# Optimization experiments

Measured on AMD Instinct MI355X. Metric: run time of the kernel, lower is better.

Reference implementation:

```python
import jax, jax.numpy as jnp
import numpy as np

N_NODES = 50000
N_EDGES = 800000
F_IN = 128
LN_EPS = 1e-5


def _linear_params(key, fan_in, fan_out):
    kw, kb = jax.random.split(key)
    w = jax.random.normal(kw, (fan_in, fan_out), dtype=jnp.float32) * 0.02
    b = jax.random.normal(kb, (fan_out,), dtype=jnp.float32) * 0.02
    return w, b


def setup_inputs() -> dict:
    key = jax.random.key(0)
    ks = jax.random.split(key, 16)
    x = jax.random.normal(ks[0], (N_NODES, F_IN), dtype=jnp.float32)
    edge_index = jax.random.randint(ks[1], (2, N_EDGES), 0, N_NODES, dtype=jnp.int32)
    w1a, b1a = _linear_params(ks[2], F_IN, 256)
    w1b, b1b = _linear_params(ks[3], 256, 256)
    w2a, b2a = _linear_params(ks[4], 256, 512)
    w2b, b2b = _linear_params(ks[5], 512, 512)
    w3a, b3a = _linear_params(ks[6], 512, 1024)
    w3b, b3b = _linear_params(ks[7], 1024, 1024)
    rp1_w, rp1_b = _linear_params(ks[8], F_IN, 256)
    rp2_w, rp2_b = _linear_params(ks[9], 256, 512)
    rp3_w, rp3_b = _linear_params(ks[10], 512, 1024)
    ln1_g = jnp.ones((256,), jnp.float32); ln1_b = jnp.zeros((256,), jnp.float32)
    ln2_g = jnp.ones((512,), jnp.float32); ln2_b = jnp.zeros((512,), jnp.float32)
    ln3_g = jnp.ones((1024,), jnp.float32); ln3_b = jnp.zeros((1024,), jnp.float32)
    return dict(x=x, edge_index=edge_index,
                w1a=w1a, b1a=b1a, w1b=w1b, b1b=b1b,
                w2a=w2a, b2a=b2a, w2b=w2b, b2b=b2b,
                w3a=w3a, b3a=b3a, w3b=w3b, b3b=b3b,
                rp1_w=rp1_w, rp1_b=rp1_b, rp2_w=rp2_w, rp2_b=rp2_b,
                rp3_w=rp3_w, rp3_b=rp3_b,
                ln1_g=ln1_g, ln1_b=ln1_b, ln2_g=ln2_g, ln2_b=ln2_b,
                ln3_g=ln3_g, ln3_b=ln3_b)


def _layer_norm(h, g, b):
    mu = jnp.mean(h, axis=-1, keepdims=True)
    var = jnp.mean(jnp.square(h - mu), axis=-1, keepdims=True)
    return (h - mu) * jax.lax.rsqrt(var + LN_EPS) * g + b


def _gin_conv(h, src, dst, wa, ba, wb, bb):
    # GINConv with eps=0: mlp(x_i + sum_{j->i} x_j), scatter-add at targets
    agg = jax.ops.segment_sum(h[src], dst, num_segments=N_NODES)
    z = h + agg
    z = jax.nn.relu(z @ wa + ba)
    z = jax.nn.relu(z @ wb + bb)
    return z


def _forward(x, edge_index,
             w1a, b1a, w1b, b1b, w2a, b2a, w2b, b2b, w3a, b3a, w3b, b3b,
             rp1_w, rp1_b, rp2_w, rp2_b, rp3_w, rp3_b,
             ln1_g, ln1_b, ln2_g, ln2_b, ln3_g, ln3_b):
    src, dst = edge_index[0], edge_index[1]
    # block 1
    res = x @ rp1_w + rp1_b
    h = _gin_conv(x, src, dst, w1a, b1a, w1b, b1b)
    h = jax.nn.relu(h + res)          # dropout = identity in eval
    h = _layer_norm(h, ln1_g, ln1_b)
    # block 2
    res = h @ rp2_w + rp2_b
    h2 = _gin_conv(h, src, dst, w2a, b2a, w2b, b2b)
    h = jax.nn.relu(h2 + res)
    h = _layer_norm(h, ln2_g, ln2_b)
    # block 3
    res = h @ rp3_w + rp3_b
    h3 = _gin_conv(h, src, dst, w3a, b3a, w3b, b3b)
    h = jax.nn.relu(h3 + res)
    h = _layer_norm(h, ln3_g, ln3_b)
    return h


def reference(x, edge_index,
              w1a, b1a, w1b, b1b, w2a, b2a, w2b, b2b, w3a, b3a, w3b, b3b,
              rp1_w, rp1_b, rp2_w, rp2_b, rp3_w, rp3_b,
              ln1_g, ln1_b, ln2_g, ln2_b, ln3_g, ln3_b):
    return _forward(x, edge_index,
                    w1a, b1a, w1b, b1b, w2a, b2a, w2b, b2b, w3a, b3a, w3b, b3b,
                    rp1_w, rp1_b, rp2_w, rp2_b, rp3_w, rp3_b,
                    ln1_g, ln1_b, ln2_g, ln2_b, ln3_g, ln3_b)
```

## Files before the change

kernel.cpp:

```cpp
#include <hip/hip_runtime.h>
#include <stdint.h>

#define NN 50000
#define NE 800000
#define M_PAD 50048

typedef __attribute__((ext_vector_type(8))) short short8;
typedef __attribute__((ext_vector_type(4))) float f32x4;

static __device__ __forceinline__ float bf2f(unsigned short v) {
    union { unsigned u; float f; } c; c.u = ((unsigned)v) << 16; return c.f;
}
static __device__ __forceinline__ unsigned short f2bf(float f) {
    union { float f; unsigned u; } c; c.f = f;
    unsigned u = c.u;
    u += 0x7fffu + ((u >> 16) & 1u);
    return (unsigned short)(u >> 16);
}

__global__ void f32_to_bf16_k(const float* __restrict__ in, unsigned short* __restrict__ out, long n4) {
    long i = (long)blockIdx.x * 256 + threadIdx.x;
    if (i >= n4) return;
    float4 v = ((const float4*)in)[i];
    ushort4 o; o.x = f2bf(v.x); o.y = f2bf(v.y); o.z = f2bf(v.z); o.w = f2bf(v.w);
    ((ushort4*)out)[i] = o;
}
__global__ void wt_k(const float* __restrict__ w, unsigned short* __restrict__ wt, int K, int N) {
    int i = blockIdx.x * 256 + threadIdx.x;
    if (i >= K * N) return;
    int k = i % K, n = i / K;
    wt[i] = f2bf(w[(long)k * N + n]);
}

__global__ void zero_k(int* __restrict__ p, int n) {
    int i = blockIdx.x * 256 + threadIdx.x;
    if (i < n) p[i] = 0;
}
__global__ void hist_k(const int* __restrict__ ei, int* __restrict__ deg) {
    int e = blockIdx.x * 256 + threadIdx.x;
    if (e >= NE) return;
    atomicAdd(&deg[ei[NE + e]], 1);
}
__global__ __launch_bounds__(1024)
void scan_k(const int* __restrict__ deg, int* __restrict__ row_ptr, int* __restrict__ cursor) {
    constexpr int T = 1024, C = (NN + T - 1) / T;
    const int tid = threadIdx.x;
    const int base = tid * C;
    int s = 0;
#pragma unroll 4
    for (int i = 0; i < C; ++i) {
        int idx = base + i;
        if (idx < NN) s += deg[idx];
    }
    __shared__ int sm[T];
    sm[tid] = s;
    __syncthreads();
    for (int off = 1; off < T; off <<= 1) {
        int v = (tid >= off) ? sm[tid - off] : 0;
        __syncthreads();
        sm[tid] += v;
        __syncthreads();
    }
    int run = (tid == 0) ? 0 : sm[tid - 1];
#pragma unroll 4
    for (int i = 0; i < C; ++i) {
        int idx = base + i;
        if (idx < NN) {
            row_ptr[idx] = run;
            cursor[idx] = run;
            run += deg[idx];
        }
    }
}
__global__ void build_col_k(const int* __restrict__ ei, int* __restrict__ cursor, int* __restrict__ col) {
    int e = blockIdx.x * 256 + threadIdx.x;
    if (e >= NE) return;
    int d = ei[NE + e];
    int p = atomicAdd(&cursor[d], 1);
    col[p] = ei[e];
}

template <int V> struct VecT;
template <> struct VecT<2> { using T = unsigned int; };
template <> struct VecT<4> { using T = uint2; };
template <> struct VecT<8> { using T = uint4; };

template <int D>
__global__ __launch_bounds__(256)
void agg_gather_k(const unsigned short* __restrict__ h,
                  const int* __restrict__ row_ptr, const int* __restrict__ deg,
                  const int* __restrict__ col, unsigned short* __restrict__ z) {
    constexpr int V = D / 64;
    using VT = typename VecT<V>::T;
    union U { VT v; unsigned short s[V]; };
    const int node = blockIdx.x * 4 + (threadIdx.x >> 6);
    if (node >= NN) return;
    const int lane = threadIdx.x & 63;
    const size_t fb = (size_t)lane * V;

    float acc[V];
    {
        U b; b.v = *(const VT*)(h + (size_t)node * D + fb);
#pragma unroll
        for (int i = 0; i < V; ++i) acc[i] = bf2f(b.s[i]);
    }
    const int s = row_ptr[node];
    const int e = s + deg[node];
    int t = s;
    for (; t + 2 <= e; t += 2) {
        int s0 = col[t], s1 = col[t + 1];
        U a0, a1;
        a0.v = *(const VT*)(h + (size_t)s0 * D + fb);
        a1.v = *(const VT*)(h + (size_t)s1 * D + fb);
#pragma unroll
        for (int i = 0; i < V; ++i) acc[i] += bf2f(a0.s[i]);
#pragma unroll
        for (int i = 0; i < V; ++i) acc[i] += bf2f(a1.s[i]);
    }
    if (t < e) {
        U a; a.v = *(const VT*)(h + (size_t)col[t] * D + fb);
#pragma unroll
        for (int i = 0; i < V; ++i) acc[i] += bf2f(a.s[i]);
    }
    U o;
#pragma unroll
    for (int i = 0; i < V; ++i) o.s[i] = f2bf(acc[i]);
    *(VT*)(z + (size_t)node * D + fb) = o.v;
}

static __device__ __forceinline__ void stage_tile128x64(
    const unsigned short* __restrict__ src, size_t rstride,
    unsigned short* lds, int wid, int lane) {
#pragma unroll
    for (int r = 0; r < 4; ++r) {
        const int rows8 = wid * 32 + r * 8;
        const int row = rows8 + (lane >> 3);
        const int kblk = (lane & 7) ^ (row & 7);
        __builtin_amdgcn_global_load_lds(
            (const __attribute__((address_space(1))) void*)(src + (size_t)row * rstride + (size_t)kblk * 8),
            (__attribute__((address_space(3))) void*)(lds + rows8 * 64),
            16, 0, 0);
    }
}

#define GEMM_IDS(NT)                                                      \
    const int tid = threadIdx.x;                                          \
    const int lane = tid & 63;                                            \
    const int wid = tid >> 6;                                             \
    const int wm = wid & 1, wn = wid >> 1;                                \
    const int l15 = lane & 15, quad = lane >> 4;                          \
    int m0, n0;                                                           \
    {                                                                     \
        const int nwg = (int)(gridDim.x * gridDim.y);                     \
        const int orig = (int)(blockIdx.y * gridDim.x + blockIdx.x);      \
        const int q = nwg >> 3, r = nwg & 7;                              \
        const int xcd = orig & 7, idx = orig >> 3;                        \
        const int logical =                                               \
            (xcd < r ? xcd * (q + 1) : r * (q + 1) + (xcd - r) * q) + idx;\
        m0 = (logical / (NT)) * 128;                                      \
        n0 = (logical % (NT)) * 128;                                      \
    }

#define GEMM_KSTEP(AP, BP, KS)                                                        \
    for (int k0 = 0; k0 < (KS); k0 += 64) {                                           \
        stage_tile128x64((AP) + (size_t)m0 * (KS) + k0, (KS), lA, wid, lane);         \
        stage_tile128x64((BP) + (size_t)n0 * (KS) + k0, (KS), lB, wid, lane);         \
        __syncthreads();                                                              \
        _Pragma("unroll")                                                             \
        for (int kk = 0; kk < 2; ++kk) {                                              \
            short8 aF[4], bF[4];                                                      \
            _Pragma("unroll")                                                         \
            for (int i = 0; i < 4; ++i) {                                             \
                int ml = wm * 64 + i * 16 + l15;                                      \
                int kb = kk * 4 + quad;                                               \
                aF[i] = *(const short8*)&lA[(ml * 8 + (kb ^ (ml & 7))) * 8];          \
                int nl = wn * 64 + i * 16 + l15;                                      \
                bF[i] = *(const short8*)&lB[(nl * 8 + (kb ^ (nl & 7))) * 8];          \
            }                                                                         \
            _Pragma("unroll")                                                         \
            for (int i = 0; i < 4; ++i)                                               \
                _Pragma("unroll")                                                     \
                for (int j = 0; j < 4; ++j)                                           \
                    acc[i][j] = __builtin_amdgcn_mfma_f32_16x16x32_bf16(              \
                        aF[i], bF[j], acc[i][j], 0, 0, 0);                            \
        }                                                                             \
        __syncthreads();                                                              \
    }

template <int K, int N>
__global__ __launch_bounds__(256, 2)
void gemm_relu_k(const unsigned short* __restrict__ A, const unsigned short* __restrict__ Bt,
                 const float* __restrict__ bias, unsigned short* __restrict__ outH, int M) {
    __shared__ unsigned short lA[128 * 64];
    __shared__ unsigned short lB[128 * 64];
    GEMM_IDS(N / 128)
    f32x4 acc[4][4];
#pragma unroll
    for (int i = 0; i < 4; ++i)
#pragma unroll
        for (int j = 0; j < 4; ++j) acc[i][j] = (f32x4){0.f, 0.f, 0.f, 0.f};

    GEMM_KSTEP(A, Bt, K)

#pragma unroll
    for (int i = 0; i < 4; ++i) {
#pragma unroll
        for (int j = 0; j < 4; ++j) {
            int col = n0 + wn * 64 + j * 16 + l15;
            float bv = bias[col];
#pragma unroll
            for (int r = 0; r < 4; ++r) {
                int row = m0 + wm * 64 + i * 16 + quad * 4 + r;
                if (row < M)
                    outH[(size_t)row * N + col] = f2bf(fmaxf(acc[i][j][r] + bv, 0.f));
            }
        }
    }
}

template <int K1, int K2, int N>
__global__ __launch_bounds__(256, 2)
void gemm_fused_k(const unsigned short* __restrict__ A1, const unsigned short* __restrict__ B1t,
                  const float* __restrict__ b1,
                  const unsigned short* __restrict__ A2, const unsigned short* __restrict__ B2t,
                  const float* __restrict__ b2,
                  float* __restrict__ outF, int M) {
    __shared__ unsigned short lA[128 * 64];
    __shared__ unsigned short lB[128 * 64];
    GEMM_IDS(N / 128)
    f32x4 acc[4][4];
#pragma unroll
    for (int i = 0; i < 4; ++i)
#pragma unroll
        for (int j = 0; j < 4; ++j) acc[i][j] = (f32x4){0.f, 0.f, 0.f, 0.f};

    GEMM_KSTEP(A1, B1t, K1)

#pragma unroll
    for (int j = 0; j < 4; ++j) {
        float bv = b1[n0 + wn * 64 + j * 16 + l15];
#pragma unroll
        for (int i = 0; i < 4; ++i)
#pragma unroll
            for (int r = 0; r < 4; ++r)
                acc[i][j][r] = fmaxf(acc[i][j][r] + bv, 0.f);
    }

    GEMM_KSTEP(A2, B2t, K2)

#pragma unroll
    for (int i = 0; i < 4; ++i) {
#pragma unroll
        for (int j = 0; j < 4; ++j) {
            int col = n0 + wn * 64 + j * 16 + l15;
            float bv = b2[col];
#pragma unroll
            for (int r = 0; r < 4; ++r) {
                int row = m0 + wm * 64 + i * 16 + quad * 4 + r;
                if (row < M)
                    outF[(size_t)row * N + col] = fmaxf(acc[i][j][r] + bv, 0.f);
            }
        }
    }
}

template <int D, bool BF16OUT>
__global__ __launch_bounds__(256)
void ln_k(const float* __restrict__ t, const float* __restrict__ g, const float* __restrict__ b,
          unsigned short* __restrict__ outH, float* __restrict__ outF) {
    constexpr int VPT = D / 256;
    const int row = blockIdx.x;
    const int tid = threadIdx.x;
    const float* tp = t + (size_t)row * D;
    float vals[VPT];
    float s = 0.f, ss = 0.f;
#pragma unroll
    for (int i = 0; i < VPT; ++i) {
        float v = tp[i * 256 + tid];
        vals[i] = v; s += v; ss += v * v;
    }
#pragma unroll
    for (int off = 32; off; off >>= 1) { s += __shfl_down(s, off); ss += __shfl_down(ss, off); }
    __shared__ float ps[4], pss[4];
    int lane = tid & 63, wv = tid >> 6;
    if (lane == 0) { ps[wv] = s; pss[wv] = ss; }
    __syncthreads();
    float st = ps[0] + ps[1] + ps[2] + ps[3];
    float sst = pss[0] + pss[1] + pss[2] + pss[3];
    float mean = st / D;
    float var = sst / D - mean * mean;
    float inv = rsqrtf(var + 1e-5f);
#pragma unroll
    for (int i = 0; i < VPT; ++i) {
        int c = i * 256 + tid;
        float o = (vals[i] - mean) * inv * g[c] + b[c];
        if (BF16OUT) outH[(size_t)row * D + c] = f2bf(o);
        else outF[(size_t)row * D + c] = o;
    }
}

static inline int cdiv(long a, long b) { return (int)((a + b - 1) / b); }

extern "C" void kernel_launch(void* const* d_in, const int* in_sizes, int n_in,
                              void* d_out, int out_size, void* d_ws, size_t ws_size,
                              hipStream_t stream) {
    const float* x   = (const float*)d_in[0];
    const int*   ei  = (const int*)  d_in[1];
    const float* w1a = (const float*)d_in[2],  *b1a = (const float*)d_in[3];
    const float* w1b = (const float*)d_in[4],  *b1b = (const float*)d_in[5];
    const float* w2a = (const float*)d_in[6],  *b2a = (const float*)d_in[7];
    const float* w2b = (const float*)d_in[8],  *b2b = (const float*)d_in[9];
    const float* w3a = (const float*)d_in[10], *b3a = (const float*)d_in[11];
    const float* w3b = (const float*)d_in[12], *b3b = (const float*)d_in[13];
    const float* rp1 = (const float*)d_in[14], *rp1b = (const float*)d_in[15];
    const float* rp2 = (const float*)d_in[16], *rp2b = (const float*)d_in[17];
    const float* rp3 = (const float*)d_in[18], *rp3b = (const float*)d_in[19];
    const float* g1 = (const float*)d_in[20], *be1 = (const float*)d_in[21];
    const float* g2 = (const float*)d_in[22], *be2 = (const float*)d_in[23];
    const float* g3 = (const float*)d_in[24], *be3 = (const float*)d_in[25];

    char* ws = (char*)d_ws;
    size_t off = 0;
    auto alloc = [&](size_t n) { char* p = ws + off; off += (n + 255) & ~(size_t)255; return p; };
    unsigned short* w1aT = (unsigned short*)alloc((size_t)128 * 256 * 2);
    unsigned short* w1bT = (unsigned short*)alloc((size_t)256 * 256 * 2);
    unsigned short* w2aT = (unsigned short*)alloc((size_t)256 * 512 * 2);
    unsigned short* w2bT = (unsigned short*)alloc((size_t)512 * 512 * 2);
    unsigned short* w3aT = (unsigned short*)alloc((size_t)512 * 1024 * 2);
    unsigned short* w3bT = (unsigned short*)alloc((size_t)1024 * 1024 * 2);
    unsigned short* rp1T = (unsigned short*)alloc((size_t)128 * 256 * 2);
    unsigned short* rp2T = (unsigned short*)alloc((size_t)256 * 512 * 2);
    unsigned short* rp3T = (unsigned short*)alloc((size_t)512 * 1024 * 2);
    unsigned short* hA  = (unsigned short*)alloc((size_t)M_PAD * 512 * 2);
    unsigned short* hB  = (unsigned short*)alloc((size_t)M_PAD * 512 * 2);
    unsigned short* zin = (unsigned short*)alloc((size_t)M_PAD * 512 * 2);
    unsigned short* z1  = (unsigned short*)alloc((size_t)M_PAD * 1024 * 2);
    float* resb = (float*)alloc((size_t)M_PAD * 1024 * 4);
    int* deg     = (int*)alloc((size_t)NN * 4);
    int* row_ptr = (int*)alloc((size_t)NN * 4);
    int* cursor  = (int*)alloc((size_t)NN * 4);
    int* colv    = (int*)alloc((size_t)NE * 4);
    (void)ws_size; (void)in_sizes; (void)n_in; (void)out_size;

    zero_k<<<cdiv(NN, 256), 256, 0, stream>>>(deg, NN);
    hist_k<<<cdiv(NE, 256), 256, 0, stream>>>(ei, deg);
    scan_k<<<1, 1024, 0, stream>>>(deg, row_ptr, cursor);
    build_col_k<<<cdiv(NE, 256), 256, 0, stream>>>(ei, cursor, colv);

    wt_k<<<cdiv(128 * 256, 256), 256, 0, stream>>>(w1a, w1aT, 128, 256);
    wt_k<<<cdiv(256 * 256, 256), 256, 0, stream>>>(w1b, w1bT, 256, 256);
    wt_k<<<cdiv(256 * 512, 256), 256, 0, stream>>>(w2a, w2aT, 256, 512);
    wt_k<<<cdiv(512 * 512, 256), 256, 0, stream>>>(w2b, w2bT, 512, 512);
    wt_k<<<cdiv(512 * 1024, 256), 256, 0, stream>>>(w3a, w3aT, 512, 1024);
    wt_k<<<cdiv(1024 * 1024, 256), 256, 0, stream>>>(w3b, w3bT, 1024, 1024);
    wt_k<<<cdiv(128 * 256, 256), 256, 0, stream>>>(rp1, rp1T, 128, 256);
    wt_k<<<cdiv(256 * 512, 256), 256, 0, stream>>>(rp2, rp2T, 256, 512);
    wt_k<<<cdiv(512 * 1024, 256), 256, 0, stream>>>(rp3, rp3T, 512, 1024);

    f32_to_bf16_k<<<cdiv((long)NN * 128 / 4, 256), 256, 0, stream>>>(x, hA, (long)NN * 128 / 4);

    agg_gather_k<128><<<cdiv(NN, 4), 256, 0, stream>>>(hA, row_ptr, deg, colv, zin);
    gemm_relu_k<128, 256><<<dim3(2, 391), 256, 0, stream>>>(zin, w1aT, b1a, z1, NN);
    gemm_fused_k<256, 128, 256><<<dim3(2, 391), 256, 0, stream>>>(z1, w1bT, b1b, hA, rp1T, rp1b, resb, NN);
    ln_k<256, true><<<NN, 256, 0, stream>>>(resb, g1, be1, hB, nullptr);

    agg_gather_k<256><<<cdiv(NN, 4), 256, 0, stream>>>(hB, row_ptr, deg, colv, zin);
    gemm_relu_k<256, 512><<<dim3(4, 391), 256, 0, stream>>>(zin, w2aT, b2a, z1, NN);
    gemm_fused_k<512, 256, 512><<<dim3(4, 391), 256, 0, stream>>>(z1, w2bT, b2b, hB, rp2T, rp2b, resb, NN);
    ln_k<512, true><<<NN, 256, 0, stream>>>(resb, g2, be2, hA, nullptr);

    agg_gather_k<512><<<cdiv(NN, 4), 256, 0, stream>>>(hA, row_ptr, deg, colv, zin);
    gemm_relu_k<512, 1024><<<dim3(8, 391), 256, 0, stream>>>(zin, w3aT, b3a, z1, NN);
    gemm_fused_k<1024, 512, 1024><<<dim3(8, 391), 256, 0, stream>>>(z1, w3bT, b3b, hA, rp3T, rp3b, resb, NN);
    ln_k<1024, false><<<NN, 256, 0, stream>>>(resb, g3, be3, nullptr, (float*)d_out);
}
```

Measured before the change: 1.257 ms.

## Double-buffer GEMM LDS tiles and store bf16 pre-LayerNorm activations

Replaces the single-buffered k-loop with a two-stage LDS ping-pong so the next 128x64 tiles load while MFMAs run on the current ones, with one barrier per step. The fused GEMM also gains a bf16 output mode that blocks 1 and 2 use for the residual sum, so LayerNorm reads half the bytes. Double-buffering doubles LDS use to 64KB per block, which may limit occupancy. The bf16 intermediate adds rounding before normalisation.

After: 1.417 ms. +12.8%, slower.

```diff
diff --git a/kernel.cpp b/kernel.cpp
--- a/kernel.cpp
+++ b/kernel.cpp
@@ -161,38 +161,50 @@
         n0 = (logical % (NT)) * 128;                                      \
     }
 
-#define GEMM_KSTEP(AP, BP, KS)                                                        \
-    for (int k0 = 0; k0 < (KS); k0 += 64) {                                           \
-        stage_tile128x64((AP) + (size_t)m0 * (KS) + k0, (KS), lA, wid, lane);         \
-        stage_tile128x64((BP) + (size_t)n0 * (KS) + k0, (KS), lB, wid, lane);         \
-        __syncthreads();                                                              \
-        _Pragma("unroll")                                                             \
-        for (int kk = 0; kk < 2; ++kk) {                                              \
-            short8 aF[4], bF[4];                                                      \
-            _Pragma("unroll")                                                         \
-            for (int i = 0; i < 4; ++i) {                                             \
-                int ml = wm * 64 + i * 16 + l15;                                      \
-                int kb = kk * 4 + quad;                                               \
-                aF[i] = *(const short8*)&lA[(ml * 8 + (kb ^ (ml & 7))) * 8];          \
-                int nl = wn * 64 + i * 16 + l15;                                      \
-                bF[i] = *(const short8*)&lB[(nl * 8 + (kb ^ (nl & 7))) * 8];          \
+#define GEMM_PIPE(AP, BP, KS)                                                         \
+    {                                                                                 \
+        stage_tile128x64((AP) + (size_t)m0 * (KS), (KS), &lA[0][0], wid, lane);       \
+        stage_tile128x64((BP) + (size_t)n0 * (KS), (KS), &lB[0][0], wid, lane);       \
+        asm volatile("s_waitcnt vmcnt(0)" ::: "memory");                              \
+        __builtin_amdgcn_s_barrier();                                                 \
+        const int NT_ = (KS) / 64;                                                    \
+        for (int t = 0; t < NT_; ++t) {                                               \
+            const int cb = t & 1;                                                     \
+            if (t + 1 < NT_) {                                                        \
+                stage_tile128x64((AP) + (size_t)m0 * (KS) + (size_t)(t + 1) * 64,     \
+                                 (KS), &lA[cb ^ 1][0], wid, lane);                    \
+                stage_tile128x64((BP) + (size_t)n0 * (KS) + (size_t)(t + 1) * 64,     \
+                                 (KS), &lB[cb ^ 1][0], wid, lane);                    \
             }                                                                         \
             _Pragma("unroll")                                                         \
-            for (int i = 0; i < 4; ++i)                                               \
+            for (int kk = 0; kk < 2; ++kk) {                                          \
+                short8 aF[4], bF[4];                                                  \
                 _Pragma("unroll")                                                     \
-                for (int j = 0; j < 4; ++j)                                           \
-                    acc[i][j] = __builtin_amdgcn_mfma_f32_16x16x32_bf16(              \
-                        aF[i], bF[j], acc[i][j], 0, 0, 0);                            \
+                for (int i = 0; i < 4; ++i) {                                         \
+                    int ml = wm * 64 + i * 16 + l15;                                  \
+                    int kb = kk * 4 + quad;                                           \
+                    aF[i] = *(const short8*)&lA[cb][(ml * 8 + (kb ^ (ml & 7))) * 8];  \
+                    int nl = wn * 64 + i * 16 + l15;                                  \
+                    bF[i] = *(const short8*)&lB[cb][(nl * 8 + (kb ^ (nl & 7))) * 8];  \
+                }                                                                     \
+                _Pragma("unroll")                                                     \
+                for (int i = 0; i < 4; ++i)                                           \
+                    _Pragma("unroll")                                                 \
+                    for (int j = 0; j < 4; ++j)                                       \
+                        acc[i][j] = __builtin_amdgcn_mfma_f32_16x16x32_bf16(          \
+                            aF[i], bF[j], acc[i][j], 0, 0, 0);                        \
+            }                                                                         \
+            asm volatile("s_waitcnt vmcnt(0)" ::: "memory");                          \
+            __builtin_amdgcn_s_barrier();                                             \
         }                                                                             \
-        __syncthreads();                                                              \
     }
 
 template <int K, int N>
 __global__ __launch_bounds__(256, 2)
 void gemm_relu_k(const unsigned short* __restrict__ A, const unsigned short* __restrict__ Bt,
                  const float* __restrict__ bias, unsigned short* __restrict__ outH, int M) {
-    __shared__ unsigned short lA[128 * 64];
-    __shared__ unsigned short lB[128 * 64];
+    __shared__ unsigned short lA[2][128 * 64];
+    __shared__ unsigned short lB[2][128 * 64];
     GEMM_IDS(N / 128)
     f32x4 acc[4][4];
 #pragma unroll
@@ -200,7 +212,7 @@
 #pragma unroll
         for (int j = 0; j < 4; ++j) acc[i][j] = (f32x4){0.f, 0.f, 0.f, 0.f};
 
-    GEMM_KSTEP(A, Bt, K)
+    GEMM_PIPE(A, Bt, K)
 
 #pragma unroll
     for (int i = 0; i < 4; ++i) {
@@ -218,15 +230,15 @@
     }
 }
 
-template <int K1, int K2, int N>
+template <int K1, int K2, int N, bool OUTBF16>
 __global__ __launch_bounds__(256, 2)
 void gemm_fused_k(const unsigned short* __restrict__ A1, const unsigned short* __restrict__ B1t,
                   const float* __restrict__ b1,
                   const unsigned short* __restrict__ A2, const unsigned short* __restrict__ B2t,
                   const float* __restrict__ b2,
-                  float* __restrict__ outF, int M) {
-    __shared__ unsigned short lA[128 * 64];
-    __shared__ unsigned short lB[128 * 64];
+                  unsigned short* __restrict__ outH, float* __restrict__ outF, int M) {
+    __shared__ unsigned short lA[2][128 * 64];
+    __shared__ unsigned short lB[2][128 * 64];
     GEMM_IDS(N / 128)
     f32x4 acc[4][4];
 #pragma unroll
@@ -234,19 +246,22 @@
 #pragma unroll
         for (int j = 0; j < 4; ++j) acc[i][j] = (f32x4){0.f, 0.f, 0.f, 0.f};
 
-    GEMM_KSTEP(A1, B1t, K1)
+    float bmid[4];
+#pragma unroll
+    for (int j = 0; j < 4; ++j) bmid[j] = b1[n0 + wn * 64 + j * 16 + l15];
+
+    GEMM_PIPE(A1, B1t, K1)
 
 #pragma unroll
     for (int j = 0; j < 4; ++j) {
-        float bv = b1[n0 + wn * 64 + j * 16 + l15];
 #pragma unroll
         for (int i = 0; i < 4; ++i)
 #pragma unroll
             for (int r = 0; r < 4; ++r)
-                acc[i][j][r] = fmaxf(acc[i][j][r] + bv, 0.f);
-    }
-
-    GEMM_KSTEP(A2, B2t, K2)
+                acc[i][j][r] = fmaxf(acc[i][j][r] + bmid[j], 0.f);
+    }
+
+    GEMM_PIPE(A2, B2t, K2)
 
 #pragma unroll
     for (int i = 0; i < 4; ++i) {
@@ -257,26 +272,30 @@
 #pragma unroll
             for (int r = 0; r < 4; ++r) {
                 int row = m0 + wm * 64 + i * 16 + quad * 4 + r;
-                if (row < M)
-                    outF[(size_t)row * N + col] = fmaxf(acc[i][j][r] + bv, 0.f);
+                if (row < M) {
+                    float v = fmaxf(acc[i][j][r] + bv, 0.f);
+                    if constexpr (OUTBF16) outH[(size_t)row * N + col] = f2bf(v);
+                    else                   outF[(size_t)row * N + col] = v;
+                }
             }
         }
     }
 }
 
-template <int D, bool BF16OUT>
+template <int D, bool INBF16, bool BF16OUT>
 __global__ __launch_bounds__(256)
-void ln_k(const float* __restrict__ t, const float* __restrict__ g, const float* __restrict__ b,
+void ln_k(const unsigned short* __restrict__ tH, const float* __restrict__ tF,
+          const float* __restrict__ g, const float* __restrict__ b,
           unsigned short* __restrict__ outH, float* __restrict__ outF) {
     constexpr int VPT = D / 256;
     const int row = blockIdx.x;
     const int tid = threadIdx.x;
-    const float* tp = t + (size_t)row * D;
     float vals[VPT];
     float s = 0.f, ss = 0.f;
 #pragma unroll
     for (int i = 0; i < VPT; ++i) {
-        float v = tp[i * 256 + tid];
+        int c = i * 256 + tid;
+        float v = INBF16 ? bf2f(tH[(size_t)row * D + c]) : tF[(size_t)row * D + c];
         vals[i] = v; s += v; ss += v * v;
     }
 #pragma unroll
@@ -361,16 +380,19 @@
 
     agg_gather_k<128><<<cdiv(NN, 4), 256, 0, stream>>>(hA, row_ptr, deg, colv, zin);
     gemm_relu_k<128, 256><<<dim3(2, 391), 256, 0, stream>>>(zin, w1aT, b1a, z1, NN);
-    gemm_fused_k<256, 128, 256><<<dim3(2, 391), 256, 0, stream>>>(z1, w1bT, b1b, hA, rp1T, rp1b, resb, NN);
-    ln_k<256, true><<<NN, 256, 0, stream>>>(resb, g1, be1, hB, nullptr);
+    gemm_fused_k<256, 128, 256, true><<<dim3(2, 391), 256, 0, stream>>>(
+        z1, w1bT, b1b, hA, rp1T, rp1b, zin, nullptr, NN);
+    ln_k<256, true, true><<<NN, 256, 0, stream>>>(zin, nullptr, g1, be1, hB, nullptr);
 
     agg_gather_k<256><<<cdiv(NN, 4), 256, 0, stream>>>(hB, row_ptr, deg, colv, zin);
     gemm_relu_k<256, 512><<<dim3(4, 391), 256, 0, stream>>>(zin, w2aT, b2a, z1, NN);
-    gemm_fused_k<512, 256, 512><<<dim3(4, 391), 256, 0, stream>>>(z1, w2bT, b2b, hB, rp2T, rp2b, resb, NN);
-    ln_k<512, true><<<NN, 256, 0, stream>>>(resb, g2, be2, hA, nullptr);
+    gemm_fused_k<512, 256, 512, true><<<dim3(4, 391), 256, 0, stream>>>(
+        z1, w2bT, b2b, hB, rp2T, rp2b, zin, nullptr, NN);
+    ln_k<512, true, true><<<NN, 256, 0, stream>>>(zin, nullptr, g2, be2, hA, nullptr);
 
     agg_gather_k<512><<<cdiv(NN, 4), 256, 0, stream>>>(hA, row_ptr, deg, colv, zin);
     gemm_relu_k<512, 1024><<<dim3(8, 391), 256, 0, stream>>>(zin, w3aT, b3a, z1, NN);
-    gemm_fused_k<1024, 512, 1024><<<dim3(8, 391), 256, 0, stream>>>(z1, w3bT, b3b, hA, rp3T, rp3b, resb, NN);
-    ln_k<1024, false><<<NN, 256, 0, stream>>>(resb, g3, be3, nullptr, (float*)d_out);
-}
+    gemm_fused_k<1024, 512, 1024, false><<<dim3(8, 391), 256, 0, stream>>>(
+        z1, w3bT, b3b, hA, rp3T, rp3b, nullptr, resb, NN);
+    ln_k<1024, false, false><<<NN, 256, 0, stream>>>(nullptr, resb, g3, be3, nullptr, (float*)d_out);
+}
```

## Store pre-LN residual in bf16 for early blocks, vectorize LN and tiled weight transpose

Applied to the files above, without the earlier changes.

Blocks 1 and 2 now write the fused GEMM output as bf16 into a reused buffer instead of fp32, and layer norm reads bf16 input. This halves the intermediate traffic between GEMM and LN. LN loads and stores are vectorized per thread over contiguous columns. Weight transposes use a shared-memory 32x32 tile so both reads and writes are coalesced, and the mid bias is loaded before the first K loop. Rounding the pre-LN values to bf16 adds some precision loss.

Result: no change. 1.268 ms (+0.9%).

```diff
diff --git a/kernel.cpp b/kernel.cpp
--- a/kernel.cpp
+++ b/kernel.cpp
@@ -25,11 +25,18 @@
     ushort4 o; o.x = f2bf(v.x); o.y = f2bf(v.y); o.z = f2bf(v.z); o.w = f2bf(v.w);
     ((ushort4*)out)[i] = o;
 }
-__global__ void wt_k(const float* __restrict__ w, unsigned short* __restrict__ wt, int K, int N) {
-    int i = blockIdx.x * 256 + threadIdx.x;
-    if (i >= K * N) return;
-    int k = i % K, n = i / K;
-    wt[i] = f2bf(w[(long)k * N + n]);
+__global__ __launch_bounds__(256)
+void wt_k(const float* __restrict__ w, unsigned short* __restrict__ wt, int K, int N) {
+    __shared__ unsigned short t[32][33];
+    const int bk = blockIdx.y * 32, bn = blockIdx.x * 32;
+    const int tx = threadIdx.x & 31, ty = threadIdx.x >> 5;
+#pragma unroll
+    for (int r = 0; r < 32; r += 8)
+        t[ty + r][tx] = f2bf(w[(size_t)(bk + ty + r) * N + bn + tx]);
+    __syncthreads();
+#pragma unroll
+    for (int r = 0; r < 32; r += 8)
+        wt[(size_t)(bn + ty + r) * K + bk + tx] = t[tx][ty + r];
 }
 
 __global__ void zero_k(int* __restrict__ p, int n) {
@@ -218,13 +225,13 @@
     }
 }
 
-template <int K1, int K2, int N>
+template <int K1, int K2, int N, bool OUTBF16>
 __global__ __launch_bounds__(256, 2)
 void gemm_fused_k(const unsigned short* __restrict__ A1, const unsigned short* __restrict__ B1t,
                   const float* __restrict__ b1,
                   const unsigned short* __restrict__ A2, const unsigned short* __restrict__ B2t,
                   const float* __restrict__ b2,
-                  float* __restrict__ outF, int M) {
+                  unsigned short* __restrict__ outH, float* __restrict__ outF, int M) {
     __shared__ unsigned short lA[128 * 64];
     __shared__ unsigned short lB[128 * 64];
     GEMM_IDS(N / 128)
@@ -234,16 +241,19 @@
 #pragma unroll
         for (int j = 0; j < 4; ++j) acc[i][j] = (f32x4){0.f, 0.f, 0.f, 0.f};
 
+    float bmid[4];
+#pragma unroll
+    for (int j = 0; j < 4; ++j) bmid[j] = b1[n0 + wn * 64 + j * 16 + l15];
+
     GEMM_KSTEP(A1, B1t, K1)
 
 #pragma unroll
     for (int j = 0; j < 4; ++j) {
-        float bv = b1[n0 + wn * 64 + j * 16 + l15];
 #pragma unroll
         for (int i = 0; i < 4; ++i)
 #pragma unroll
             for (int r = 0; r < 4; ++r)
-                acc[i][j][r] = fmaxf(acc[i][j][r] + bv, 0.f);
+                acc[i][j][r] = fmaxf(acc[i][j][r] + bmid[j], 0.f);
     }
 
     GEMM_KSTEP(A2, B2t, K2)
@@ -257,28 +267,44 @@
 #pragma unroll
             for (int r = 0; r < 4; ++r) {
                 int row = m0 + wm * 64 + i * 16 + quad * 4 + r;
-                if (row < M)
-                    outF[(size_t)row * N + col] = fmaxf(acc[i][j][r] + bv, 0.f);
+                if (row < M) {
+                    float v = fmaxf(acc[i][j][r] + bv, 0.f);
+                    if constexpr (OUTBF16) outH[(size_t)row * N + col] = f2bf(v);
+                    else                   outF[(size_t)row * N + col] = v;
+                }
             }
         }
     }
 }
 
-template <int D, bool BF16OUT>
+template <int D, bool INBF16, bool BF16OUT>
 __global__ __launch_bounds__(256)
-void ln_k(const float* __restrict__ t, const float* __restrict__ g, const float* __restrict__ b,
+void ln_k(const unsigned short* __restrict__ tH, const float* __restrict__ tF,
+          const float* __restrict__ g, const float* __restrict__ b,
           unsigned short* __restrict__ outH, float* __restrict__ outF) {
     constexpr int VPT = D / 256;
     const int row = blockIdx.x;
     const int tid = threadIdx.x;
-    const float* tp = t + (size_t)row * D;
+    const int c0 = tid * VPT;
     float vals[VPT];
+    if constexpr (INBF16) {
+        const unsigned short* p = tH + (size_t)row * D + c0;
+        if constexpr (VPT == 1) { vals[0] = bf2f(p[0]); }
+        else if constexpr (VPT == 2) {
+            ushort2 u = *(const ushort2*)p; vals[0] = bf2f(u.x); vals[1] = bf2f(u.y);
+        } else {
+            ushort4 u = *(const ushort4*)p;
+            vals[0] = bf2f(u.x); vals[1] = bf2f(u.y); vals[2] = bf2f(u.z); vals[3] = bf2f(u.w);
+        }
+    } else {
+        const float* p = tF + (size_t)row * D + c0;
+        if constexpr (VPT == 1) { vals[0] = p[0]; }
+        else if constexpr (VPT == 2) { float2 u = *(const float2*)p; vals[0] = u.x; vals[1] = u.y; }
+        else { float4 u = *(const float4*)p; vals[0] = u.x; vals[1] = u.y; vals[2] = u.z; vals[3] = u.w; }
+    }
     float s = 0.f, ss = 0.f;
 #pragma unroll
-    for (int i = 0; i < VPT; ++i) {
-        float v = tp[i * 256 + tid];
-        vals[i] = v; s += v; ss += v * v;
-    }
+    for (int i = 0; i < VPT; ++i) { s += vals[i]; ss += vals[i] * vals[i]; }
 #pragma unroll
     for (int off = 32; off; off >>= 1) { s += __shfl_down(s, off); ss += __shfl_down(ss, off); }
     __shared__ float ps[4], pss[4];
@@ -290,12 +316,24 @@
     float mean = st / D;
     float var = sst / D - mean * mean;
     float inv = rsqrtf(var + 1e-5f);
-#pragma unroll
-    for (int i = 0; i < VPT; ++i) {
-        int c = i * 256 + tid;
-        float o = (vals[i] - mean) * inv * g[c] + b[c];
-        if (BF16OUT) outH[(size_t)row * D + c] = f2bf(o);
-        else outF[(size_t)row * D + c] = o;
+    float outv[VPT];
+#pragma unroll
+    for (int i = 0; i < VPT; ++i)
+        outv[i] = (vals[i] - mean) * inv * g[c0 + i] + b[c0 + i];
+    if constexpr (BF16OUT) {
+        unsigned short* p = outH + (size_t)row * D + c0;
+        if constexpr (VPT == 1) { p[0] = f2bf(outv[0]); }
+        else if constexpr (VPT == 2) {
+            ushort2 u; u.x = f2bf(outv[0]); u.y = f2bf(outv[1]); *(ushort2*)p = u;
+        } else {
+            ushort4 u; u.x = f2bf(outv[0]); u.y = f2bf(outv[1]); u.z = f2bf(outv[2]); u.w = f2bf(outv[3]);
+            *(ushort4*)p = u;
+        }
+    } else {
+        float* p = outF + (size_t)row * D + c0;
+        if constexpr (VPT == 1) { p[0] = outv[0]; }
+        else if constexpr (VPT == 2) { float2 u; u.x = outv[0]; u.y = outv[1]; *(float2*)p = u; }
+        else { float4 u; u.x = outv[0]; u.y = outv[1]; u.z = outv[2]; u.w = outv[3]; *(float4*)p = u; }
     }
 }
 
@@ -347,30 +385,33 @@
     scan_k<<<1, 1024, 0, stream>>>(deg, row_ptr, cursor);
     build_col_k<<<cdiv(NE, 256), 256, 0, stream>>>(ei, cursor, colv);
 
-    wt_k<<<cdiv(128 * 256, 256), 256, 0, stream>>>(w1a, w1aT, 128, 256);
-    wt_k<<<cdiv(256 * 256, 256), 256, 0, stream>>>(w1b, w1bT, 256, 256);
-    wt_k<<<cdiv(256 * 512, 256), 256, 0, stream>>>(w2a, w2aT, 256, 512);
-    wt_k<<<cdiv(512 * 512, 256), 256, 0, stream>>>(w2b, w2bT, 512, 512);
-    wt_k<<<cdiv(512 * 1024, 256), 256, 0, stream>>>(w3a, w3aT, 512, 1024);
-    wt_k<<<cdiv(1024 * 1024, 256), 256, 0, stream>>>(w3b, w3bT, 1024, 1024);
-    wt_k<<<cdiv(128 * 256, 256), 256, 0, stream>>>(rp1, rp1T, 128, 256);
-    wt_k<<<cdiv(256 * 512, 256), 256, 0, stream>>>(rp2, rp2T, 256, 512);
-    wt_k<<<cdiv(512 * 1024, 256), 256, 0, stream>>>(rp3, rp3T, 512, 1024);
+    wt_k<<<dim3(256 / 32, 128 / 32), 256, 0, stream>>>(w1a, w1aT, 128, 256);
+    wt_k<<<dim3(256 / 32, 256 / 32), 256, 0, stream>>>(w1b, w1bT, 256, 256);
+    wt_k<<<dim3(512 / 32, 256 / 32), 256, 0, stream>>>(w2a, w2aT, 256, 512);
+    wt_k<<<dim3(512 / 32, 512 / 32), 256, 0, stream>>>(w2b, w2bT, 512, 512);
+    wt_k<<<dim3(1024 / 32, 512 / 32), 256, 0, stream>>>(w3a, w3aT, 512, 1024);
+    wt_k<<<dim3(1024 / 32, 1024 / 32), 256, 0, stream>>>(w3b, w3bT, 1024, 1024);
+    wt_k<<<dim3(256 / 32, 128 / 32), 256, 0, stream>>>(rp1, rp1T, 128, 256);
+    wt_k<<<dim3(512 / 32, 256 / 32), 256, 0, stream>>>(rp2, rp2T, 256, 512);
+    wt_k<<<dim3(1024 / 32, 512 / 32), 256, 0, stream>>>(rp3, rp3T, 512, 1024);
 
     f32_to_bf16_k<<<cdiv((long)NN * 128 / 4, 256), 256, 0, stream>>>(x, hA, (long)NN * 128 / 4);
 
     agg_gather_k<128><<<cdiv(NN, 4), 256, 0, stream>>>(hA, row_ptr, deg, colv, zin);
     gemm_relu_k<128, 256><<<dim3(2, 391), 256, 0, stream>>>(zin, w1aT, b1a, z1, NN);
-    gemm_fused_k<256, 128, 256><<<dim3(2, 391), 256, 0, stream>>>(z1, w1bT, b1b, hA, rp1T, rp1b, resb, NN);
-    ln_k<256, true><<<NN, 256, 0, stream>>>(resb, g1, be1, hB, nullptr);
+    gemm_fused_k<256, 128, 256, true><<<dim3(2, 391), 256, 0, stream>>>(
+        z1, w1bT, b1b, hA, rp1T, rp1b, zin, nullptr, NN);
+    ln_k<256, true, true><<<NN, 256, 0, stream>>>(zin, nullptr, g1, be1, hB, nullptr);
 
     agg_gather_k<256><<<cdiv(NN, 4), 256, 0, stream>>>(hB, row_ptr, deg, colv, zin);
     gemm_relu_k<256, 512><<<dim3(4, 391), 256, 0, stream>>>(zin, w2aT, b2a, z1, NN);
-    gemm_fused_k<512, 256, 512><<<dim3(4, 391), 256, 0, stream>>>(z1, w2bT, b2b, hB, rp2T, rp2b, resb, NN);
-    ln_k<512, true><<<NN, 256, 0, stream>>>(resb, g2, be2, hA, nullptr);
+    gemm_fused_k<512, 256, 512, true><<<dim3(4, 391), 256, 0, stream>>>(
+        z1, w2bT, b2b, hB, rp2T, rp2b, zin, nullptr, NN);
+    ln_k<512, true, true><<<NN, 256, 0, stream>>>(zin, nullptr, g2, be2, hA, nullptr);
 
     agg_gather_k<512><<<cdiv(NN, 4), 256, 0, stream>>>(hA, row_ptr, deg, colv, zin);
     gemm_relu_k<512, 1024><<<dim3(8, 391), 256, 0, stream>>>(zin, w3aT, b3a, z1, NN);
-    gemm_fused_k<1024, 512, 1024><<<dim3(8, 391), 256, 0, stream>>>(z1, w3bT, b3b, hA, rp3T, rp3b, resb, NN);
-    ln_k<1024, false><<<NN, 256, 0, stream>>>(resb, g3, be3, nullptr, (float*)d_out);
-}
+    gemm_fused_k<1024, 512, 1024, false><<<dim3(8, 391), 256, 0, stream>>>(
+        z1, w3bT, b3b, hA, rp3T, rp3b, nullptr, resb, NN);
+    ln_k<1024, false, false><<<NN, 256, 0, stream>>>(nullptr, resb, g3, be3, nullptr, (float*)d_out);
+}
```
